# Performance work log

Measured on AMD Instinct MI355X. Metric: run time of the kernel, lower is better.

The kernel has to match this reference:

```python
import jax, jax.numpy as jnp
import numpy as np

H = 4                      # attention heads
L_NAMES = ['self', 'cross'] * 3
K_LIST = [None, None, 128, 128, 64, 64]  # top-k per layer (None = full attention)
BN_EPS = 1e-5


def conv1d(x, W, b):
    # 1x1 Conv1d: x [B, Ci, N], W [Co, Ci], b [Co]
    return jnp.einsum('oi,bin->bon', W, x) + b[:, None]


def bn_eval(x, g, b):
    # BatchNorm1d in eval mode with running mean 0 / var 1
    inv = 1.0 / np.sqrt(1.0 + BN_EPS)
    return (g * inv)[:, None] * x + b[:, None]


def mha(x, src, Wq, bq, Wk, bk, Wv, bv, Wm, bm, k):
    B, D, N = x.shape
    dh = D // H
    q = conv1d(x, Wq, bq).reshape(B, dh, H, N)
    kk = conv1d(src, Wk, bk).reshape(B, dh, H, -1)
    v = conv1d(src, Wv, bv).reshape(B, dh, H, -1)
    scores = jnp.einsum('bdhn,bdhm->bhnm', q, kk) / np.sqrt(dh)  # [B,H,N,M]
    if k is None:
        p = jax.nn.softmax(scores, axis=-1)
        out = jnp.einsum('bhnm,bdhm->bdhn', p, v)
    else:
        vals, idx = jax.lax.top_k(scores, k)          # [B,H,N,k]
        S = jax.nn.softmax(vals, axis=-1)
        # gather value vectors at the top-k key indices: [B,dh,H,N,k]
        vg = jnp.take_along_axis(v[:, :, :, None, :], idx[:, None, :, :, :], axis=4)
        out = jnp.einsum('bhnk,bdhnk->bdhn', S, vg)
    return conv1d(out.reshape(B, D, N), Wm, bm)


def log_ot(scores, alpha, iters):
    b, m, n = scores.shape
    bins0 = jnp.broadcast_to(alpha, (b, m, 1))
    bins1 = jnp.broadcast_to(alpha, (b, 1, n))
    a = jnp.broadcast_to(alpha, (b, 1, 1))
    Z0 = jnp.concatenate([jnp.concatenate([scores, bins0], -1),
                          jnp.concatenate([bins1, a], -1)], 1)  # [b,m+1,n+1]
    norm = -np.log(float(m + n))
    log_mu = jnp.concatenate([jnp.full((m,), norm, scores.dtype),
                              jnp.array([np.log(float(n)) + norm], scores.dtype)])
    log_nu = jnp.concatenate([jnp.full((n,), norm, scores.dtype),
                              jnp.array([np.log(float(m)) + norm], scores.dtype)])
    log_mu = jnp.broadcast_to(log_mu, (b, m + 1))
    log_nu = jnp.broadcast_to(log_nu, (b, n + 1))

    def step(carry, _):
        u, v = carry
        u = log_mu - jax.nn.logsumexp(Z0 + v[:, None, :], axis=2)
        v = log_nu - jax.nn.logsumexp(Z0 + u[:, :, None], axis=1)
        return (u, v), None

    (u, v), _ = jax.lax.scan(step, (jnp.zeros_like(log_mu), jnp.zeros_like(log_nu)),
                             None, length=iters)
    return Z0 + u[:, :, None] + v[:, None, :] - norm


def _forward(desc0, desc1, Wq, bq, Wk, bk, Wv, bv, Wm, bm,
             W1, b1, g1, be1, W2, b2, Wf, bf, alpha, iters):
    d0, d1 = desc0, desc1
    for i, (name, k) in enumerate(zip(L_NAMES, K_LIST)):
        s0, s1 = (d1, d0) if name == 'cross' else (d0, d1)

        def prop(x, src):
            msg = mha(x, src, Wq[i], bq[i], Wk[i], bk[i], Wv[i], bv[i], Wm[i], bm[i], k)
            h = jnp.concatenate([x, msg], axis=1)           # [B, 2D, N]
            h = jax.nn.relu(bn_eval(conv1d(h, W1[i], b1[i]), g1[i], be1[i]))
            return conv1d(h, W2[i], b2[i])

        dlt0, dlt1 = prop(d0, s0), prop(d1, s1)
        d0, d1 = d0 + dlt0, d1 + dlt1
    m0 = conv1d(d0, Wf, bf)
    m1 = conv1d(d1, Wf, bf)
    scores = jnp.einsum('bdn,bdm->bnm', m0, m1) / np.sqrt(m0.shape[1])
    return log_ot(scores, alpha, iters)


def setup_inputs() -> dict:
    B, D, N, L = 4, 128, 1024, 6
    key = jax.random.key(0)
    ks = jax.random.split(key, 20)

    def nrm(k, shape, s):
        return jax.random.normal(k, shape, jnp.float32) * s

    sw = 1.0 / np.sqrt(D)
    return {
        'desc0': nrm(ks[0], (B, D, N), 1.0),
        'desc1': nrm(ks[1], (B, D, N), 1.0),
        'Wq': nrm(ks[2], (L, D, D), sw), 'bq': jnp.zeros((L, D), jnp.float32),
        'Wk': nrm(ks[3], (L, D, D), sw), 'bk': jnp.zeros((L, D), jnp.float32),
        'Wv': nrm(ks[4], (L, D, D), sw), 'bv': jnp.zeros((L, D), jnp.float32),
        'Wm': nrm(ks[5], (L, D, D), sw), 'bm': jnp.zeros((L, D), jnp.float32),
        'W1': nrm(ks[6], (L, 2 * D, 2 * D), 1.0 / np.sqrt(2 * D)),
        'b1': jnp.zeros((L, 2 * D), jnp.float32),
        'g1': jnp.ones((L, 2 * D), jnp.float32),
        'be1': jnp.zeros((L, 2 * D), jnp.float32),
        'W2': nrm(ks[7], (L, D, 2 * D), 1.0 / np.sqrt(2 * D)),
        'b2': jnp.zeros((L, D), jnp.float32),
        'Wf': nrm(ks[8], (D, D), sw), 'bf': jnp.zeros((D,), jnp.float32),
        'alpha': jnp.asarray(1.0, jnp.float32),
        'iters': 20,
    }


def reference(desc0, desc1, Wq, bq, Wk, bk, Wv, bv, Wm, bm,
              W1, b1, g1, be1, W2, b2, Wf, bf, alpha, iters):
    return _forward(desc0, desc1, Wq, bq, Wk, bk, Wv, bv, Wm, bm,
                    W1, b1, g1, be1, W2, b2, Wf, bf, alpha, iters)
```

## Files before the change

kernel.cpp:

```cpp
#include <hip/hip_runtime.h>
#include <stdint.h>

#define NPOS   1024
#define DMODEL 128
#define NP1    1025
#define PLP    1053700
#define PSTR   1028
#define NORMF  (-7.624618986159398f)
#define LOGN   (6.931471805599453f)

typedef __attribute__((ext_vector_type(8))) short s8v;
typedef __attribute__((ext_vector_type(4))) float f4v;
typedef unsigned short ushort_t;

#define MFMA(a, b, c) __builtin_amdgcn_mfma_f32_16x16x32_bf16((a), (b), (c), 0, 0, 0)

static __device__ __forceinline__ ushort_t f2bf(float f) {
    union { float f; uint32_t u; } c; c.f = f;
    uint32_t u = c.u;
    return (ushort_t)((u + 0x7fffu + ((u >> 16) & 1u)) >> 16);
}

#define NW0 294912
#define NW1 98304
#define NW2 393216
#define NW3 196608
#define NW4 16384
#define NB5 2304
__global__ __launch_bounds__(256) void prep_weights(
    const float* __restrict__ Wq, const float* __restrict__ Wk, const float* __restrict__ Wv,
    const float* __restrict__ bq, const float* __restrict__ bk, const float* __restrict__ bv,
    const float* __restrict__ Wm, const float* __restrict__ W1, const float* __restrict__ W2,
    const float* __restrict__ Wf,
    ushort_t* __restrict__ wqkv, ushort_t* __restrict__ wm, ushort_t* __restrict__ w1,
    ushort_t* __restrict__ w2, ushort_t* __restrict__ wf, float* __restrict__ bqkv)
{
    int idx = blockIdx.x * 256 + threadIdx.x;
    if (idx < NW0) {
        int l = idx / 49152, r2 = idx % 49152;
        int r = r2 / 128, i = r2 % 128;
        int sel = r >> 7, rr = r & 127;
        int o = ((rr & 31) << 2) + (rr >> 5);
        const float* src = sel == 0 ? Wq : (sel == 1 ? Wk : Wv);
        wqkv[idx] = f2bf(src[((size_t)l * 128 + o) * 128 + i]);
        return;
    }
    idx -= NW0;
    if (idx < NW1) {
        int l = idx / 16384, o = (idx % 16384) / 128, ip = idx % 128;
        int i = ((ip & 31) << 2) + (ip >> 5);
        wm[idx] = f2bf(Wm[((size_t)l * 128 + o) * 128 + i]);
        return;
    }
    idx -= NW1;
    if (idx < NW2) { w1[idx] = f2bf(W1[idx]); return; }
    idx -= NW2;
    if (idx < NW3) { w2[idx] = f2bf(W2[idx]); return; }
    idx -= NW3;
    if (idx < NW4) { wf[idx] = f2bf(Wf[idx]); return; }
    idx -= NW4;
    if (idx < NB5) {
        int l = idx / 384, r = idx % 384;
        int sel = r >> 7, rr = r & 127;
        int o = ((rr & 31) << 2) + (rr >> 5);
        const float* src = sel == 0 ? bq : (sel == 1 ? bk : bv);
        bqkv[idx] = src[l * 128 + o];
    }
}

__global__ __launch_bounds__(256) void transpose_in(
    const float* __restrict__ desc0, const float* __restrict__ desc1,
    float* __restrict__ df, ushort_t* __restrict__ db)
{
    int g = blockIdx.z;
    int nb = blockIdx.x << 6, cb = blockIdx.y << 5;
    __shared__ float sm[32][65];
    const float* S = (g < 4 ? desc0 : desc1);
    int gl = g & 3;
    {
        int row = threadIdx.x >> 3, c8 = (threadIdx.x & 7) << 3;
        const float* p = S + ((size_t)gl * 128 + cb + row) * NPOS + nb + c8;
        float4 v0 = *(const float4*)p;
        float4 v1 = *(const float4*)(p + 4);
        sm[row][c8 + 0] = v0.x; sm[row][c8 + 1] = v0.y; sm[row][c8 + 2] = v0.z; sm[row][c8 + 3] = v0.w;
        sm[row][c8 + 4] = v1.x; sm[row][c8 + 5] = v1.y; sm[row][c8 + 6] = v1.z; sm[row][c8 + 7] = v1.w;
    }
    __syncthreads();
    int n = threadIdx.x >> 2, cc = (threadIdx.x & 3) << 3;
    float y[8];
    #pragma unroll
    for (int e = 0; e < 8; ++e) y[e] = sm[cc + e][n];
    size_t base = ((size_t)g * NPOS + nb + n) * DMODEL + cb + cc;
    *(float4*)(df + base) = make_float4(y[0], y[1], y[2], y[3]);
    *(float4*)(df + base + 4) = make_float4(y[4], y[5], y[6], y[7]);
    s8v o;
    #pragma unroll
    for (int e = 0; e < 8; ++e) o[e] = (short)f2bf(y[e]);
    *(s8v*)(db + base) = o;
}

__global__ __launch_bounds__(256) void conv_mfma(
    const ushort_t* __restrict__ X0, const ushort_t* __restrict__ X1, int c0, int Ci,
    const ushort_t* __restrict__ W, const float* __restrict__ bias,
    const float* __restrict__ bn_g, const float* __restrict__ bn_b,
    float* __restrict__ resid, ushort_t* __restrict__ outb, int Co, int mode)
{
    int g = blockIdx.z;
    int nb = blockIdx.x << 6;
    int obb = blockIdx.y << 6;
    int wave = threadIdx.x >> 6, lane = threadIdx.x & 63;
    int lrow = lane & 15, lk = (lane >> 4) << 3;
    int ob = obb + (wave << 4);
    f4v acc[4] = {};
    const ushort_t* wrow = W + (size_t)(ob + lrow) * Ci + lk;
    for (int k0 = 0; k0 < Ci; k0 += 32) {
        int k = k0 + lk;
        s8v b = *(const s8v*)(wrow + k0);
        #pragma unroll
        for (int t = 0; t < 4; ++t) {
            int n = nb + (t << 4) + lrow;
            const ushort_t* xp;
            if (k < c0) xp = X0 + ((size_t)g * NPOS + n) * c0 + k;
            else        xp = X1 + ((size_t)g * NPOS + n) * (Ci - c0) + (k - c0);
            s8v a = *(const s8v*)xp;
            acc[t] = MFMA(a, b, acc[t]);
        }
    }
    __shared__ float sm[64][68];
    #pragma unroll
    for (int t = 0; t < 4; ++t)
        #pragma unroll
        for (int r = 0; r < 4; ++r)
            sm[(t << 4) + ((lane >> 4) << 2) + r][(wave << 4) + lrow] = acc[t][r];
    __syncthreads();
    const float BN_INV = 0.9999950000374997f;
    int n = threadIdx.x >> 2, oc = (threadIdx.x & 3) << 4;
    int o0 = obb + oc;
    float y[16];
    #pragma unroll
    for (int e = 0; e < 16; ++e) y[e] = sm[n][oc + e] + bias[o0 + e];
    size_t base = ((size_t)g * NPOS + nb + n) * Co + o0;
    if (mode == 1) {
        #pragma unroll
        for (int e = 0; e < 16; ++e)
            y[e] = fmaxf(bn_g[o0 + e] * BN_INV * y[e] + bn_b[o0 + e], 0.f);
    } else if (mode == 2) {
        float* rp = resid + base;
        #pragma unroll
        for (int q = 0; q < 16; q += 4) {
            float4 r4 = *(const float4*)(rp + q);
            y[q] += r4.x; y[q + 1] += r4.y; y[q + 2] += r4.z; y[q + 3] += r4.w;
            *(float4*)(rp + q) = make_float4(y[q], y[q + 1], y[q + 2], y[q + 3]);
        }
    }
    s8v o1, o2;
    #pragma unroll
    for (int e = 0; e < 8; ++e) { o1[e] = (short)f2bf(y[e]); o2[e] = (short)f2bf(y[8 + e]); }
    *(s8v*)(outb + base) = o1;
    *(s8v*)(outb + base + 8) = o2;
}

__global__ __launch_bounds__(256) void qkv_mfma(
    const ushort_t* __restrict__ X, const ushort_t* __restrict__ W,
    const float* __restrict__ bias,
    ushort_t* __restrict__ Qb, ushort_t* __restrict__ Kb, ushort_t* __restrict__ Vb)
{
    int g = blockIdx.z;
    int nb = blockIdx.x << 6;
    int obb = blockIdx.y << 6;
    int wave = threadIdx.x >> 6, lane = threadIdx.x & 63;
    int lrow = lane & 15, lk = (lane >> 4) << 3;
    int ob = obb + (wave << 4);
    f4v acc[4] = {};
    const ushort_t* wrow = W + (size_t)(ob + lrow) * DMODEL + lk;
    for (int k0 = 0; k0 < DMODEL; k0 += 32) {
        s8v b = *(const s8v*)(wrow + k0);
        #pragma unroll
        for (int t = 0; t < 4; ++t) {
            int n = nb + (t << 4) + lrow;
            s8v a = *(const s8v*)(X + ((size_t)g * NPOS + n) * DMODEL + k0 + lk);
            acc[t] = MFMA(a, b, acc[t]);
        }
    }
    __shared__ float sm[64][68];
    #pragma unroll
    for (int t = 0; t < 4; ++t)
        #pragma unroll
        for (int r = 0; r < 4; ++r)
            sm[(t << 4) + ((lane >> 4) << 2) + r][(wave << 4) + lrow] = acc[t][r];
    __syncthreads();
    if (obb < 256) {
        int n = threadIdx.x >> 2, oc = (threadIdx.x & 3) << 4;
        int ov = obb + oc;
        ushort_t* dst = (ov < 128) ? Qb : Kb;
        int c = ov & 127;
        float y[16];
        #pragma unroll
        for (int e = 0; e < 16; ++e) y[e] = sm[n][oc + e] + bias[ov + e];
        size_t base = ((size_t)g * NPOS + nb + n) * DMODEL + c;
        s8v o1, o2;
        #pragma unroll
        for (int e = 0; e < 8; ++e) { o1[e] = (short)f2bf(y[e]); o2[e] = (short)f2bf(y[8 + e]); }
        *(s8v*)(dst + base) = o1;
        *(s8v*)(dst + base + 8) = o2;
    } else {
        int c = threadIdx.x >> 2, mc = (threadIdx.x & 3) << 4;
        float bc = bias[obb + c];
        float y[16];
        #pragma unroll
        for (int e = 0; e < 16; ++e) y[e] = sm[mc + e][c] + bc;
        size_t base = ((size_t)g * DMODEL + (obb - 256) + c) * NPOS + nb + mc;
        s8v o1, o2;
        #pragma unroll
        for (int e = 0; e < 8; ++e) { o1[e] = (short)f2bf(y[e]); o2[e] = (short)f2bf(y[8 + e]); }
        *(s8v*)(Vb + base) = o1;
        *(s8v*)(Vb + base + 8) = o2;
    }
}

__global__ __launch_bounds__(512) void attn_fused(
    const ushort_t* __restrict__ Qb, const ushort_t* __restrict__ Kb,
    const ushort_t* __restrict__ Vb, ushort_t* __restrict__ ao,
    int k, int cross)
{
    __shared__ ushort_t sc[32 * 1024];
    int gh = blockIdx.y;
    int g = gh >> 2, h = gh & 3;
    int g2 = cross ? (g ^ 4) : g;
    int n0 = blockIdx.x << 5;
    int wave = threadIdx.x >> 6, lane = threadIdx.x & 63;
    int lrow = lane & 15, lq = lane >> 4;

    {
        int qg = wave >> 2, kq = wave & 3;
        s8v qa = *(const s8v*)(Qb + ((size_t)g * NPOS + n0 + (qg << 4) + lrow) * DMODEL
                               + (h << 5) + (lq << 3));
        const float scale = 0.17677669529663687f;
        int qrow = (qg << 4) + lrow;
        int swz = (qrow & 7) << 4;
        for (int mt = 0; mt < 16; ++mt) {
            int m = (kq << 8) + (mt << 4);
            s8v kb = *(const s8v*)(Kb + ((size_t)g2 * NPOS + m + lrow) * DMODEL
                                   + (h << 5) + (lq << 3));
            f4v z = {};
            z = MFMA(kb, qa, z);
            uint32_t p0 = (uint32_t)f2bf(z[0] * scale) | ((uint32_t)f2bf(z[1] * scale) << 16);
            uint32_t p1 = (uint32_t)f2bf(z[2] * scale) | ((uint32_t)f2bf(z[3] * scale) << 16);
            int byte = ((qrow << 11) + ((m + (lq << 2)) << 1)) ^ swz;
            *(uint2*)((char*)sc + byte) = make_uint2(p0, p1);
        }
    }
    __syncthreads();

    {
        bool dosel = (k < NPOS);
        for (int rr = 0; rr < 4; ++rr) {
            int row = (wave << 2) + rr;
            int swz = (row & 7) << 4;
            int base = (row << 11) + (lane << 5);
            uint4 d0 = *(const uint4*)((const char*)sc + (base ^ swz));
            uint4 d1 = *(const uint4*)((const char*)sc + ((base + 16) ^ swz));
            uint32_t wd[8] = {d0.x, d0.y, d0.z, d0.w, d1.x, d1.y, d1.z, d1.w};
            unsigned u[16];
            float val[16];
            #pragma unroll
            for (int q = 0; q < 8; ++q) {
                unsigned r0 = wd[q] & 0xFFFFu, r1 = wd[q] >> 16;
                union { unsigned ui; float f; } c0, c1;
                c0.ui = r0 << 16; c1.ui = r1 << 16;
                val[2 * q] = c0.f; val[2 * q + 1] = c1.f;
                u[2 * q]     = r0 ^ ((r0 >> 15) ? 0xFFFFu : 0x8000u);
                u[2 * q + 1] = r1 ^ ((r1 >> 15) ? 0xFFFFu : 0x8000u);
            }
            float mx = val[0];
            #pragma unroll
            for (int t = 1; t < 16; ++t) mx = fmaxf(mx, val[t]);
            #pragma unroll
            for (int o = 32; o; o >>= 1) mx = fmaxf(mx, __shfl_xor(mx, o));

            bool sel[16];
            if (dosel) {
                unsigned prefix = 0;
                bool exact = false;
                for (int bit = 15; bit >= 0 && !exact; --bit) {
                    unsigned cand = prefix | (1u << bit);
                    int c = 0;
                    #pragma unroll
                    for (int t = 0; t < 16; ++t)
                        c += __popcll(__ballot(u[t] >= cand));
                    if (c >= k) { prefix = cand; exact = (c == k); }
                }
                if (exact) {
                    #pragma unroll
                    for (int t = 0; t < 16; ++t) sel[t] = (u[t] >= prefix);
                } else {
                    int cgt = 0;
                    #pragma unroll
                    for (int t = 0; t < 16; ++t)
                        cgt += __popcll(__ballot(u[t] > prefix));
                    int need = k - cgt;
                    unsigned long long lmask = (1ull << lane) - 1ull;
                    int before = 0;
                    #pragma unroll
                    for (int t = 0; t < 16; ++t)
                        before += __popcll(__ballot(u[t] == prefix) & lmask);
                    int loc = 0;
                    #pragma unroll
                    for (int t = 0; t < 16; ++t) {
                        bool tie = (u[t] == prefix);
                        sel[t] = (u[t] > prefix) || (tie && (before + loc < need));
                        loc += tie ? 1 : 0;
                    }
                }
            } else {
                #pragma unroll
                for (int t = 0; t < 16; ++t) sel[t] = true;
            }
            float w[16], sum = 0.f;
            #pragma unroll
            for (int t = 0; t < 16; ++t) {
                w[t] = sel[t] ? __expf(val[t] - mx) : 0.f;
                sum += w[t];
            }
            #pragma unroll
            for (int o = 32; o; o >>= 1) sum += __shfl_xor(sum, o);
            float inv = 1.f / sum;
            uint32_t ow[8];
            #pragma unroll
            for (int q = 0; q < 8; ++q)
                ow[q] = (uint32_t)f2bf(w[2 * q] * inv)
                      | ((uint32_t)f2bf(w[2 * q + 1] * inv) << 16);
            *(uint4*)((char*)sc + (base ^ swz)) = make_uint4(ow[0], ow[1], ow[2], ow[3]);
            *(uint4*)((char*)sc + ((base + 16) ^ swz)) = make_uint4(ow[4], ow[5], ow[6], ow[7]);
        }
    }
    __syncthreads();

    {
        int khalf = wave >> 2, rowg = (wave >> 1) & 1, dimg = wave & 1;
        int rb = rowg << 4, db = dimg << 4;
        int prow = rb + lrow;
        int pswz = (prow & 7) << 4;
        int pbase = (prow << 11) + (khalf << 10) + (lq << 4);
        const ushort_t* vbase = Vb + ((size_t)g2 * DMODEL + (h << 5) + db + lrow) * NPOS
                                + (khalf << 9) + (lq << 3);
        f4v acc = {};
        #pragma unroll
        for (int ks = 0; ks < 16; ++ks) {
            s8v pa = *(const s8v*)((const char*)sc + ((pbase + (ks << 6)) ^ pswz));
            s8v vv = *(const s8v*)(vbase + (ks << 5));
            acc = MFMA(pa, vv, acc);
        }
        __syncthreads();
        if (khalf == 1)
            *(f4v*)((char*)sc + ((((wave & 3) << 6) + lane) << 4)) = acc;
        __syncthreads();
        if (khalf == 0) {
            f4v other = *(const f4v*)((char*)sc + (((wave << 6) + lane) << 4));
            acc = acc + other;
            #pragma unroll
            for (int r = 0; r < 4; ++r) {
                int n = n0 + rb + (lq << 2) + r;
                ao[((size_t)g * NPOS + n) * DMODEL + (h << 5) + db + lrow] = f2bf(acc[r]);
            }
        }
    }
}

__global__ __launch_bounds__(256) void final_mfma(
    const ushort_t* __restrict__ md, float* __restrict__ Z0P, float* __restrict__ Z0T)
{
    int b = blockIdx.z;
    int wave = threadIdx.x >> 6, lane = threadIdx.x & 63;
    int wr = wave >> 1, wc = wave & 1;
    int n0 = (blockIdx.y << 7) + (wr << 6);
    int m0 = (blockIdx.x << 7) + (wc << 6);
    int lrow = lane & 15, lk = (lane >> 4) << 3;
    f4v acc[4][4] = {};
    for (int k0 = 0; k0 < DMODEL; k0 += 32) {
        s8v qa[4], kb[4];
        #pragma unroll
        for (int t = 0; t < 4; ++t) {
            qa[t] = *(const s8v*)(md + ((size_t)b * NPOS + n0 + (t << 4) + lrow) * DMODEL + k0 + lk);
            kb[t] = *(const s8v*)(md + ((size_t)(b + 4) * NPOS + m0 + (t << 4) + lrow) * DMODEL + k0 + lk);
        }
        #pragma unroll
        for (int tn = 0; tn < 4; ++tn)
            #pragma unroll
            for (int tm = 0; tm < 4; ++tm)
                acc[tn][tm] = MFMA(qa[tn], kb[tm], acc[tn][tm]);
    }
    const float scf = 0.08838834764831845f;
    int rbase = (lane >> 4) << 2;
    #pragma unroll
    for (int tn = 0; tn < 4; ++tn) {
        #pragma unroll
        for (int tm = 0; tm < 4; ++tm) {
            #pragma unroll
            for (int r = 0; r < 4; ++r) {
                int n = n0 + (tn << 4) + rbase + r;
                int m = m0 + (tm << 4) + lrow;
                float y = acc[tn][tm][r] * scf;
                Z0P[(size_t)b * PLP + (size_t)n * PSTR + m] = y;
                Z0T[(size_t)b * PLP + (size_t)m * PSTR + n] = y;
            }
        }
    }
}

__global__ __launch_bounds__(1024) void ot_init(
    float* __restrict__ Z0P, float* __restrict__ Z0T, float* __restrict__ v,
    const float* __restrict__ alpha)
{
    float a = *alpha;
    int b = blockIdx.x, t = threadIdx.x;
    Z0P[(size_t)b * PLP + (size_t)t * PSTR + 1024] = a;
    Z0P[(size_t)b * PLP + (size_t)1024 * PSTR + t] = a;
    Z0T[(size_t)b * PLP + (size_t)t * PSTR + 1024] = a;
    Z0T[(size_t)b * PLP + (size_t)1024 * PSTR + t] = a;
    v[b * NP1 + t] = 0.f;
    if (t == 0) {
        Z0P[(size_t)b * PLP + (size_t)1024 * PSTR + 1024] = a;
        Z0T[(size_t)b * PLP + (size_t)1024 * PSTR + 1024] = a;
        v[b * NP1 + 1024] = 0.f;
    }
}

__global__ __launch_bounds__(256) void lse_sweep(
    const float* __restrict__ Z, const float* __restrict__ vin,
    float* __restrict__ uout)
{
    int wv = threadIdx.x >> 6, lane = threadIdx.x & 63;
    int r = blockIdx.x * 4 + wv;
    int b = r / NP1, i = r - b * NP1;
    const float* z  = Z + (size_t)b * PLP + (size_t)i * PSTR;
    const float* vb = vin + b * NP1;
    float x[17];
    #pragma unroll
    for (int t = 0; t < 4; ++t) {
        int j = ((t << 6) + lane) << 2;
        float4 zz = *(const float4*)(z + j);
        float4 vv = *(const float4*)(vb + j);
        x[4 * t + 0] = zz.x + vv.x;
        x[4 * t + 1] = zz.y + vv.y;
        x[4 * t + 2] = zz.z + vv.z;
        x[4 * t + 3] = zz.w + vv.w;
    }
    x[16] = (lane == 0) ? (z[1024] + vb[1024]) : -1e30f;
    float m = x[0];
    #pragma unroll
    for (int t = 1; t < 17; ++t) m = fmaxf(m, x[t]);
    #pragma unroll
    for (int o = 32; o; o >>= 1) m = fmaxf(m, __shfl_xor(m, o));
    float sum = 0.f;
    #pragma unroll
    for (int t = 0; t < 17; ++t) sum += __expf(x[t] - m);
    #pragma unroll
    for (int o = 32; o; o >>= 1) sum += __shfl_xor(sum, o);
    if (lane == 0)
        uout[b * NP1 + i] = NORMF + ((i == 1024) ? LOGN : 0.f) - (m + __logf(sum));
}

__global__ __launch_bounds__(256) void ot_final(
    float* __restrict__ out, const float* __restrict__ Z0P,
    const float* __restrict__ u, const float* __restrict__ v)
{
    int r = blockIdx.x;
    int b = r / NP1, i = r - b * NP1;
    float ui = u[b * NP1 + i] - NORMF;
    const float* zp = Z0P + (size_t)b * PLP + (size_t)i * PSTR;
    float* zo = out + ((size_t)b * NP1 + i) * NP1;
    const float* vb = v + b * NP1;
    for (int j = threadIdx.x; j < NP1; j += 256) zo[j] = zp[j] + ui + vb[j];
}

extern "C" void kernel_launch(void* const* d_in, const int* in_sizes, int n_in,
                              void* d_out, int out_size, void* d_ws, size_t ws_size,
                              hipStream_t stream)
{
    (void)in_sizes; (void)n_in; (void)out_size; (void)ws_size;
    const float* desc0 = (const float*)d_in[0];
    const float* desc1 = (const float*)d_in[1];
    const float* Wq = (const float*)d_in[2];  const float* bq = (const float*)d_in[3];
    const float* Wk = (const float*)d_in[4];  const float* bk = (const float*)d_in[5];
    const float* Wv = (const float*)d_in[6];  const float* bv = (const float*)d_in[7];
    const float* Wm = (const float*)d_in[8];  const float* bm = (const float*)d_in[9];
    const float* W1 = (const float*)d_in[10]; const float* b1 = (const float*)d_in[11];
    const float* g1 = (const float*)d_in[12]; const float* be1 = (const float*)d_in[13];
    const float* W2 = (const float*)d_in[14]; const float* b2 = (const float*)d_in[15];
    const float* Wf = (const float*)d_in[16]; const float* bf = (const float*)d_in[17];
    const float* alpha = (const float*)d_in[18];

    float* Zout = (float*)d_out;
    float* ws = (float*)d_ws;
    size_t o = 0;
    float* d_f32      = ws;                          o += 1048576;
    ushort_t* d_bf    = (ushort_t*)(ws + o);         o += 524288;
    ushort_t* Qb      = (ushort_t*)(ws + o);         o += 524288;
    ushort_t* Kb      = (ushort_t*)(ws + o);         o += 524288;
    ushort_t* Vb      = (ushort_t*)(ws + o);         o += 524288;
    ushort_t* aob     = (ushort_t*)(ws + o);         o += 524288;
    ushort_t* msgb    = (ushort_t*)(ws + o);         o += 524288;
    ushort_t* hb      = (ushort_t*)(ws + o);         o += 1048576;
    ushort_t* mdesc   = (ushort_t*)(ws + o);         o += 524288;
    ushort_t* wqkv    = (ushort_t*)(ws + o);         o += 147456;
    ushort_t* wmw     = (ushort_t*)(ws + o);         o += 49152;
    ushort_t* w1w     = (ushort_t*)(ws + o);         o += 196608;
    ushort_t* w2w     = (ushort_t*)(ws + o);         o += 98304;
    ushort_t* wfw     = (ushort_t*)(ws + o);         o += 8192;
    float* bqkv       = ws + o;                      o += 2304;
    float* ub         = ws + o;                      o += 4352;
    float* vb         = ws + o;                      o += 4352;
    float* Z0P        = ws + o;                      o += 4214800;
    float* Z0T        = ws + o;                      o += 4214800;

    dim3 blk(256);
    prep_weights<<<dim3((NW0 + NW1 + NW2 + NW3 + NW4 + NB5 + 255) / 256), blk, 0, stream>>>(
        Wq, Wk, Wv, bq, bk, bv, Wm, W1, W2, Wf, wqkv, wmw, w1w, w2w, wfw, bqkv);
    transpose_in<<<dim3(16, 4, 8), blk, 0, stream>>>(desc0, desc1, d_f32, d_bf);

    static const int KLIST[6] = {1024, 1024, 128, 128, 64, 64};
    for (int l = 0; l < 6; ++l) {
        int cross = l & 1;
        int k = KLIST[l];
        qkv_mfma<<<dim3(16, 6, 8), blk, 0, stream>>>(
            d_bf, wqkv + (size_t)l * 49152, bqkv + l * 384, Qb, Kb, Vb);
        attn_fused<<<dim3(32, 32), dim3(512), 0, stream>>>(Qb, Kb, Vb, aob, k, cross);
        conv_mfma<<<dim3(16, 2, 8), blk, 0, stream>>>(
            aob, (const ushort_t*)nullptr, 128, 128, wmw + (size_t)l * 16384,
            bm + l * 128, nullptr, nullptr, nullptr, msgb, 128, 0);
        conv_mfma<<<dim3(16, 4, 8), blk, 0, stream>>>(
            d_bf, msgb, 128, 256, w1w + (size_t)l * 65536,
            b1 + l * 256, g1 + l * 256, be1 + l * 256, nullptr, hb, 256, 1);
        conv_mfma<<<dim3(16, 2, 8), blk, 0, stream>>>(
            hb, (const ushort_t*)nullptr, 256, 256, w2w + (size_t)l * 32768,
            b2 + l * 128, nullptr, nullptr, d_f32, d_bf, 128, 2);
    }
    conv_mfma<<<dim3(16, 2, 8), blk, 0, stream>>>(
        d_bf, (const ushort_t*)nullptr, 128, 128, wfw, bf,
        nullptr, nullptr, nullptr, mdesc, 128, 0);
    final_mfma<<<dim3(8, 8, 4), blk, 0, stream>>>(mdesc, Z0P, Z0T);
    ot_init<<<dim3(4), dim3(1024), 0, stream>>>(Z0P, Z0T, vb, alpha);
    for (int it = 0; it < 20; ++it) {
        lse_sweep<<<dim3(1025), blk, 0, stream>>>(Z0P, vb, ub);
        lse_sweep<<<dim3(1025), blk, 0, stream>>>(Z0T, ub, vb);
    }
    ot_final<<<dim3(4100), blk, 0, stream>>>(Zout, Z0P, ub, vb);
}
```

Measured before the change: 820.4 us.

## Halve attention block size, use packed bf16 convert, compare top-k on floats

```diff
diff --git a/kernel.cpp b/kernel.cpp
--- a/kernel.cpp
+++ b/kernel.cpp
@@ -19,6 +19,11 @@
     union { float f; uint32_t u; } c; c.f = f;
     uint32_t u = c.u;
     return (ushort_t)((u + 0x7fffu + ((u >> 16) & 1u)) >> 16);
+}
+static __device__ __forceinline__ uint32_t cvtpk(float lo, float hi) {
+    uint32_t r;
+    asm("v_cvt_pk_bf16_f32 %0, %1, %2" : "=v"(r) : "v"(lo), "v"(hi));
+    return r;
 }
 
 #define NW0 294912
@@ -93,10 +98,9 @@
     size_t base = ((size_t)g * NPOS + nb + n) * DMODEL + cb + cc;
     *(float4*)(df + base) = make_float4(y[0], y[1], y[2], y[3]);
     *(float4*)(df + base + 4) = make_float4(y[4], y[5], y[6], y[7]);
-    s8v o;
-    #pragma unroll
-    for (int e = 0; e < 8; ++e) o[e] = (short)f2bf(y[e]);
-    *(s8v*)(db + base) = o;
+    uint4 pk = make_uint4(cvtpk(y[0], y[1]), cvtpk(y[2], y[3]),
+                          cvtpk(y[4], y[5]), cvtpk(y[6], y[7]));
+    *(uint4*)(db + base) = pk;
 }
 
 __global__ __launch_bounds__(256) void conv_mfma(
@@ -153,11 +157,12 @@
             *(float4*)(rp + q) = make_float4(y[q], y[q + 1], y[q + 2], y[q + 3]);
         }
     }
-    s8v o1, o2;
-    #pragma unroll
-    for (int e = 0; e < 8; ++e) { o1[e] = (short)f2bf(y[e]); o2[e] = (short)f2bf(y[8 + e]); }
-    *(s8v*)(outb + base) = o1;
-    *(s8v*)(outb + base + 8) = o2;
+    uint4 p0 = make_uint4(cvtpk(y[0], y[1]), cvtpk(y[2], y[3]),
+                          cvtpk(y[4], y[5]), cvtpk(y[6], y[7]));
+    uint4 p1 = make_uint4(cvtpk(y[8], y[9]), cvtpk(y[10], y[11]),
+                          cvtpk(y[12], y[13]), cvtpk(y[14], y[15]));
+    *(uint4*)(outb + base) = p0;
+    *(uint4*)(outb + base + 8) = p1;
 }
 
 __global__ __launch_bounds__(256) void qkv_mfma(
@@ -198,11 +203,12 @@
         #pragma unroll
         for (int e = 0; e < 16; ++e) y[e] = sm[n][oc + e] + bias[ov + e];
         size_t base = ((size_t)g * NPOS + nb + n) * DMODEL + c;
-        s8v o1, o2;
-        #pragma unroll
-        for (int e = 0; e < 8; ++e) { o1[e] = (short)f2bf(y[e]); o2[e] = (short)f2bf(y[8 + e]); }
-        *(s8v*)(dst + base) = o1;
-        *(s8v*)(dst + base + 8) = o2;
+        uint4 p0 = make_uint4(cvtpk(y[0], y[1]), cvtpk(y[2], y[3]),
+                              cvtpk(y[4], y[5]), cvtpk(y[6], y[7]));
+        uint4 p1 = make_uint4(cvtpk(y[8], y[9]), cvtpk(y[10], y[11]),
+                              cvtpk(y[12], y[13]), cvtpk(y[14], y[15]));
+        *(uint4*)(dst + base) = p0;
+        *(uint4*)(dst + base + 8) = p1;
     } else {
         int c = threadIdx.x >> 2, mc = (threadIdx.x & 3) << 4;
         float bc = bias[obb + c];
@@ -210,43 +216,43 @@
         #pragma unroll
         for (int e = 0; e < 16; ++e) y[e] = sm[mc + e][c] + bc;
         size_t base = ((size_t)g * DMODEL + (obb - 256) + c) * NPOS + nb + mc;
-        s8v o1, o2;
-        #pragma unroll
-        for (int e = 0; e < 8; ++e) { o1[e] = (short)f2bf(y[e]); o2[e] = (short)f2bf(y[8 + e]); }
-        *(s8v*)(Vb + base) = o1;
-        *(s8v*)(Vb + base + 8) = o2;
-    }
-}
-
-__global__ __launch_bounds__(512) void attn_fused(
+        uint4 p0 = make_uint4(cvtpk(y[0], y[1]), cvtpk(y[2], y[3]),
+                              cvtpk(y[4], y[5]), cvtpk(y[6], y[7]));
+        uint4 p1 = make_uint4(cvtpk(y[8], y[9]), cvtpk(y[10], y[11]),
+                              cvtpk(y[12], y[13]), cvtpk(y[14], y[15]));
+        *(uint4*)(Vb + base) = p0;
+        *(uint4*)(Vb + base + 8) = p1;
+    }
+}
+
+__global__ __launch_bounds__(256) void attn_fused(
     const ushort_t* __restrict__ Qb, const ushort_t* __restrict__ Kb,
     const ushort_t* __restrict__ Vb, ushort_t* __restrict__ ao,
     int k, int cross)
 {
-    __shared__ ushort_t sc[32 * 1024];
+    __shared__ ushort_t sc[16 * 1024];
     int gh = blockIdx.y;
     int g = gh >> 2, h = gh & 3;
     int g2 = cross ? (g ^ 4) : g;
-    int n0 = blockIdx.x << 5;
+    int n0 = blockIdx.x << 4;
     int wave = threadIdx.x >> 6, lane = threadIdx.x & 63;
     int lrow = lane & 15, lq = lane >> 4;
 
     {
-        int qg = wave >> 2, kq = wave & 3;
-        s8v qa = *(const s8v*)(Qb + ((size_t)g * NPOS + n0 + (qg << 4) + lrow) * DMODEL
+        int kq = wave;
+        s8v qa = *(const s8v*)(Qb + ((size_t)g * NPOS + n0 + lrow) * DMODEL
                                + (h << 5) + (lq << 3));
         const float scale = 0.17677669529663687f;
-        int qrow = (qg << 4) + lrow;
-        int swz = (qrow & 7) << 4;
+        int swz = (lrow & 7) << 4;
         for (int mt = 0; mt < 16; ++mt) {
             int m = (kq << 8) + (mt << 4);
             s8v kb = *(const s8v*)(Kb + ((size_t)g2 * NPOS + m + lrow) * DMODEL
                                    + (h << 5) + (lq << 3));
             f4v z = {};
             z = MFMA(kb, qa, z);
-            uint32_t p0 = (uint32_t)f2bf(z[0] * scale) | ((uint32_t)f2bf(z[1] * scale) << 16);
-            uint32_t p1 = (uint32_t)f2bf(z[2] * scale) | ((uint32_t)f2bf(z[3] * scale) << 16);
-            int byte = ((qrow << 11) + ((m + (lq << 2)) << 1)) ^ swz;
+            uint32_t p0 = cvtpk(z[0] * scale, z[1] * scale);
+            uint32_t p1 = cvtpk(z[2] * scale, z[3] * scale);
+            int byte = ((lrow << 11) + ((m + (lq << 2)) << 1)) ^ swz;
             *(uint2*)((char*)sc + byte) = make_uint2(p0, p1);
         }
     }
@@ -261,16 +267,12 @@
             uint4 d0 = *(const uint4*)((const char*)sc + (base ^ swz));
             uint4 d1 = *(const uint4*)((const char*)sc + ((base + 16) ^ swz));
             uint32_t wd[8] = {d0.x, d0.y, d0.z, d0.w, d1.x, d1.y, d1.z, d1.w};
-            unsigned u[16];
             float val[16];
             #pragma unroll
             for (int q = 0; q < 8; ++q) {
-                unsigned r0 = wd[q] & 0xFFFFu, r1 = wd[q] >> 16;
                 union { unsigned ui; float f; } c0, c1;
-                c0.ui = r0 << 16; c1.ui = r1 << 16;
+                c0.ui = wd[q] << 16; c1.ui = wd[q] & 0xFFFF0000u;
                 val[2 * q] = c0.f; val[2 * q + 1] = c1.f;
-                u[2 * q]     = r0 ^ ((r0 >> 15) ? 0xFFFFu : 0x8000u);
-                u[2 * q + 1] = r1 ^ ((r1 >> 15) ? 0xFFFFu : 0x8000u);
             }
             float mx = val[0];
             #pragma unroll
@@ -284,31 +286,37 @@
                 bool exact = false;
                 for (int bit = 15; bit >= 0 && !exact; --bit) {
                     unsigned cand = prefix | (1u << bit);
+                    unsigned craw = (cand & 0x8000u) ? (cand ^ 0x8000u) : (cand ^ 0xFFFFu);
+                    union { unsigned ui; float f; } cf; cf.ui = craw << 16;
+                    float cf_f = cf.f;
                     int c = 0;
                     #pragma unroll
                     for (int t = 0; t < 16; ++t)
-                        c += __popcll(__ballot(u[t] >= cand));
+                        c += __popcll(__ballot(val[t] >= cf_f));
                     if (c >= k) { prefix = cand; exact = (c == k); }
                 }
+                unsigned praw = (prefix & 0x8000u) ? (prefix ^ 0x8000u) : (prefix ^ 0xFFFFu);
+                union { unsigned ui; float f; } pf; pf.ui = praw << 16;
+                float thr = pf.f;
                 if (exact) {
                     #pragma unroll
-                    for (int t = 0; t < 16; ++t) sel[t] = (u[t] >= prefix);
+                    for (int t = 0; t < 16; ++t) sel[t] = (val[t] >= thr);
                 } else {
                     int cgt = 0;
                     #pragma unroll
                     for (int t = 0; t < 16; ++t)
-                        cgt += __popcll(__ballot(u[t] > prefix));
+                        cgt += __popcll(__ballot(val[t] > thr));
                     int need = k - cgt;
                     unsigned long long lmask = (1ull << lane) - 1ull;
                     int before = 0;
                     #pragma unroll
                     for (int t = 0; t < 16; ++t)
-                        before += __popcll(__ballot(u[t] == prefix) & lmask);
+                        before += __popcll(__ballot(val[t] == thr) & lmask);
                     int loc = 0;
                     #pragma unroll
                     for (int t = 0; t < 16; ++t) {
-                        bool tie = (u[t] == prefix);
-                        sel[t] = (u[t] > prefix) || (tie && (before + loc < need));
+                        bool tie = (val[t] == thr);
+                        sel[t] = (val[t] > thr) || (tie && (before + loc < need));
                         loc += tie ? 1 : 0;
                     }
                 }
@@ -328,8 +336,7 @@
             uint32_t ow[8];
             #pragma unroll
             for (int q = 0; q < 8; ++q)
-                ow[q] = (uint32_t)f2bf(w[2 * q] * inv)
-                      | ((uint32_t)f2bf(w[2 * q + 1] * inv) << 16);
+                ow[q] = cvtpk(w[2 * q] * inv, w[2 * q + 1] * inv);
             *(uint4*)((char*)sc + (base ^ swz)) = make_uint4(ow[0], ow[1], ow[2], ow[3]);
             *(uint4*)((char*)sc + ((base + 16) ^ swz)) = make_uint4(ow[4], ow[5], ow[6], ow[7]);
         }
@@ -337,11 +344,10 @@
     __syncthreads();
 
     {
-        int khalf = wave >> 2, rowg = (wave >> 1) & 1, dimg = wave & 1;
-        int rb = rowg << 4, db = dimg << 4;
-        int prow = rb + lrow;
-        int pswz = (prow & 7) << 4;
-        int pbase = (prow << 11) + (khalf << 10) + (lq << 4);
+        int khalf = wave >> 1, dimg = wave & 1;
+        int db = dimg << 4;
+        int pswz = (lrow & 7) << 4;
+        int pbase = (lrow << 11) + (khalf << 10) + (lq << 4);
         const ushort_t* vbase = Vb + ((size_t)g2 * DMODEL + (h << 5) + db + lrow) * NPOS
                                 + (khalf << 9) + (lq << 3);
         f4v acc = {};
@@ -353,14 +359,14 @@
         }
         __syncthreads();
         if (khalf == 1)
-            *(f4v*)((char*)sc + ((((wave & 3) << 6) + lane) << 4)) = acc;
+            *(f4v*)((char*)sc + (((dimg << 6) + lane) << 4)) = acc;
         __syncthreads();
         if (khalf == 0) {
-            f4v other = *(const f4v*)((char*)sc + (((wave << 6) + lane) << 4));
+            f4v other = *(const f4v*)((char*)sc + (((dimg << 6) + lane) << 4));
             acc = acc + other;
             #pragma unroll
             for (int r = 0; r < 4; ++r) {
-                int n = n0 + rb + (lq << 2) + r;
+                int n = n0 + (lq << 2) + r;
                 ao[((size_t)g * NPOS + n) * DMODEL + (h << 5) + db + lrow] = f2bf(acc[r]);
             }
         }
@@ -525,7 +531,7 @@
         int k = KLIST[l];
         qkv_mfma<<<dim3(16, 6, 8), blk, 0, stream>>>(
             d_bf, wqkv + (size_t)l * 49152, bqkv + l * 384, Qb, Kb, Vb);
-        attn_fused<<<dim3(32, 32), dim3(512), 0, stream>>>(Qb, Kb, Vb, aob, k, cross);
+        attn_fused<<<dim3(64, 32), blk, 0, stream>>>(Qb, Kb, Vb, aob, k, cross);
         conv_mfma<<<dim3(16, 2, 8), blk, 0, stream>>>(
             aob, (const ushort_t*)nullptr, 128, 128, wmw + (size_t)l * 16384,
             bm + l * 128, nullptr, nullptr, nullptr, msgb, 128, 0);
```

New measurement: 791.4 us. 1.04x faster.
